# Kernel tuning notes

Measured on AMD Instinct MI355X. Metric: run time of the kernel, lower is better.

## Reference

```python
import jax, jax.numpy as jnp
import numpy as np

N = 16384
E = 524288
F_IN, F_HID, F_OUT = 128, 256, 128
EPS = 1e-5


def setup_inputs() -> dict:
    key = jax.random.key(0)
    ks = jax.random.split(key, 8)
    x = jax.random.normal(ks[0], (N, F_IN), dtype=jnp.float32)
    edge_index = jax.random.randint(ks[1], (2, E), 0, N, dtype=jnp.int64)
    edge_weight = jax.random.uniform(ks[2], (E,), dtype=jnp.float32)
    # Linear params stored as [in, out] (y = x @ W + b; same math as torch Linear)
    W1_w = jax.random.normal(ks[3], (F_IN, F_HID), dtype=jnp.float32) / np.sqrt(F_IN)
    W1_b = jnp.zeros((F_HID,), dtype=jnp.float32)
    W2_w = jax.random.normal(ks[4], (F_HID, F_OUT), dtype=jnp.float32) / np.sqrt(F_HID)
    W2_b = jnp.zeros((F_OUT,), dtype=jnp.float32)
    ln_g = jnp.ones((F_HID,), dtype=jnp.float32)
    ln_b = jnp.zeros((F_HID,), dtype=jnp.float32)
    return {"x": x, "edge_index": edge_index, "edge_weight": edge_weight,
            "W1_w": W1_w, "W1_b": W1_b, "W2_w": W2_w, "W2_b": W2_b,
            "ln_g": ln_g, "ln_b": ln_b}


def _layernorm(h, g, b):
    mu = jnp.mean(h, axis=-1, keepdims=True)
    var = jnp.var(h, axis=-1, keepdims=True)
    return (h - mu) * jax.lax.rsqrt(var + EPS) * g + b


def reference(x, edge_index, edge_weight, W1_w, W1_b, W2_w, W2_b, ln_g, ln_b):
    n = x.shape[0]
    adj = jnp.zeros((n, n), dtype=x.dtype).at[edge_index[0], edge_index[1]].set(edge_weight)
    adj = adj + jnp.eye(n, dtype=x.dtype)
    degree = jnp.clip(adj.sum(axis=1, keepdims=True), 1.0, None)
    adj = adj / degree
    h = jnp.matmul(adj, x) @ W1_w + W1_b          # [N, F_HID]
    h = jax.nn.relu(_layernorm(h, ln_g, ln_b))
    # dropout is identity in eval mode
    out = jnp.matmul(adj, h) @ W2_w + W2_b        # [N, F_OUT]
    return out
```

## Files before the change

kernel.cpp:

```cpp
#include <hip/hip_runtime.h>

#define N_NODES 16384
#define F_IN    128
#define F_HID   256
#define F_OUT   128
#define LN_EPS  1e-5f
#define CAP     128
#define HSTR    264

typedef __attribute__((ext_vector_type(8))) short bf16x8;
typedef __attribute__((ext_vector_type(4))) float f32x4;

__device__ __forceinline__ unsigned short bf16rne(float f) {
    unsigned u = __float_as_uint(f);
    unsigned r = (u + 0x7fffu + ((u >> 16) & 1u)) >> 16;
    return (unsigned short)r;
}

__global__ void prelude_kernel(const float* __restrict__ x, unsigned short* __restrict__ xb,
                               const float* __restrict__ W1, unsigned short* __restrict__ W1t,
                               const float* __restrict__ W2, unsigned short* __restrict__ W2t,
                               int* __restrict__ cur, const unsigned* __restrict__ ei,
                               int* __restrict__ mode) {
    int b = blockIdx.x, t = threadIdx.x;
    if (b < 2048) {
        int i = (b * 256 + t) * 4;
        float4 v = *(const float4*)&x[i];
        ushort4 o;
        o.x = bf16rne(v.x); o.y = bf16rne(v.y); o.z = bf16rne(v.z); o.w = bf16rne(v.w);
        *(ushort4*)&xb[i] = o;
    } else if (b < 2176) {
        int id = (b - 2048) * 256 + t;
        int n = id >> 7, k = id & 127;
        W1t[id] = bf16rne(W1[(size_t)k * F_HID + n]);
    } else if (b < 2304) {
        int id = (b - 2176) * 256 + t;
        int n = id >> 8, k = id & 255;
        W2t[id] = bf16rne(W2[(size_t)k * F_OUT + n]);
    } else if (b < 2368) {
        cur[(b - 2304) * 256 + t] = 0;
    } else {
        __shared__ int nz;
        if (t == 0) nz = 0;
        __syncthreads();
        for (int it = 0; it < 4; ++it) {
            int idx = 2 * (t + it * 256) + 1;
            if (ei[idx] != 0u) nz = 1;
        }
        __syncthreads();
        if (t == 0) *mode = (nz == 0) ? 1 : 0;
    }
}

__global__ void fill_kernel(const void* __restrict__ ei, const int* __restrict__ mode,
                            int* __restrict__ cur, int2* __restrict__ ed, int E) {
    int base = blockIdx.x * 1024 + threadIdx.x;
    int m = *mode;
#pragma unroll
    for (int u = 0; u < 4; ++u) {
        int e = base + u * 256;
        if (e >= E) continue;
        int r, c;
        if (m) {
            const long long* p = (const long long*)ei;
            r = (int)p[e]; c = (int)p[e + E];
        } else {
            const int* p = (const int*)ei;
            r = p[e]; c = p[e + E];
        }
        int pos = atomicAdd(&cur[r], 1);
        if (pos < CAP) ed[r * CAP + pos] = make_int2(c, e);
    }
}

__global__ void dedupe_kernel(const float* __restrict__ ew, int* __restrict__ cur,
                              int2* __restrict__ ed, float* __restrict__ invdeg) {
    __shared__ int scol[4][CAP];
    __shared__ int seid[4][CAP];
    int wave = threadIdx.x >> 6, lane = threadIdx.x & 63;
    int r = blockIdx.x * 4 + wave;
    int d = cur[r];
    if (d > CAP) d = CAP;
    int2* row = ed + r * CAP;
    int mycol[2], myeid[2];
    int nown = 0;
    for (int i = lane; i < d; i += 64) {
        int2 e = row[i];
        scol[wave][i] = e.x;
        seid[wave][i] = e.y;
        mycol[nown] = e.x; myeid[nown] = e.y;
        ++nown;
    }
    __syncthreads();
    float wsum = 0.0f;
    nown = 0;
    for (int i = lane; i < d; i += 64) {
        bool kill = false;
        for (int j = 0; j < d; ++j)
            if (scol[wave][j] == mycol[nown] && seid[wave][j] > myeid[nown]) { kill = true; break; }
        float w = kill ? 0.0f : ew[myeid[nown]];
        ((int*)&row[i])[1] = __float_as_int(w);
        wsum += w;
        ++nown;
    }
    for (int off = 32; off; off >>= 1) wsum += __shfl_xor(wsum, off, 64);
    if (lane == 0) {
        invdeg[r] = 1.0f / (1.0f + wsum);
        cur[r] = d;
    }
}

__global__ void spmm_bf16_kernel(const unsigned* __restrict__ xb, const int* __restrict__ cur,
                                 const int2* __restrict__ ed, const float* __restrict__ invdeg,
                                 const float* __restrict__ bias, void* __restrict__ outp,
                                 int out_bf16) {
    int wave = threadIdx.x >> 6, lane = threadIdx.x & 63;
    int r = blockIdx.x * 4 + wave;
    const int2* row = ed + r * CAP;
    int d = cur[r];
    unsigned self = xb[r * 64 + lane];
    float ax = __uint_as_float(self << 16);
    float ay = __uint_as_float(self & 0xffff0000u);
    int j = 0;
    for (; j + 8 <= d; j += 8) {
        int2 e0 = row[j],     e1 = row[j + 1], e2 = row[j + 2], e3 = row[j + 3];
        int2 e4 = row[j + 4], e5 = row[j + 5], e6 = row[j + 6], e7 = row[j + 7];
        unsigned v0 = xb[e0.x * 64 + lane];
        unsigned v1 = xb[e1.x * 64 + lane];
        unsigned v2 = xb[e2.x * 64 + lane];
        unsigned v3 = xb[e3.x * 64 + lane];
        unsigned v4 = xb[e4.x * 64 + lane];
        unsigned v5 = xb[e5.x * 64 + lane];
        unsigned v6 = xb[e6.x * 64 + lane];
        unsigned v7 = xb[e7.x * 64 + lane];
        float w0 = __int_as_float(e0.y), w1 = __int_as_float(e1.y);
        float w2 = __int_as_float(e2.y), w3 = __int_as_float(e3.y);
        float w4 = __int_as_float(e4.y), w5 = __int_as_float(e5.y);
        float w6 = __int_as_float(e6.y), w7 = __int_as_float(e7.y);
        ax += w0 * __uint_as_float(v0 << 16) + w1 * __uint_as_float(v1 << 16)
            + w2 * __uint_as_float(v2 << 16) + w3 * __uint_as_float(v3 << 16)
            + w4 * __uint_as_float(v4 << 16) + w5 * __uint_as_float(v5 << 16)
            + w6 * __uint_as_float(v6 << 16) + w7 * __uint_as_float(v7 << 16);
        ay += w0 * __uint_as_float(v0 & 0xffff0000u) + w1 * __uint_as_float(v1 & 0xffff0000u)
            + w2 * __uint_as_float(v2 & 0xffff0000u) + w3 * __uint_as_float(v3 & 0xffff0000u)
            + w4 * __uint_as_float(v4 & 0xffff0000u) + w5 * __uint_as_float(v5 & 0xffff0000u)
            + w6 * __uint_as_float(v6 & 0xffff0000u) + w7 * __uint_as_float(v7 & 0xffff0000u);
    }
    for (; j < d; ++j) {
        int2 e = row[j];
        float w = __int_as_float(e.y);
        unsigned v = xb[e.x * 64 + lane];
        ax += w * __uint_as_float(v << 16);
        ay += w * __uint_as_float(v & 0xffff0000u);
    }
    float inv = invdeg[r];
    float ox = ax * inv, oy = ay * inv;
    if (bias) { ox += bias[2 * lane]; oy += bias[2 * lane + 1]; }
    if (out_bf16) {
        unsigned pk = ((unsigned)bf16rne(oy) << 16) | (unsigned)bf16rne(ox);
        ((unsigned*)outp)[r * 64 + lane] = pk;
    } else {
        ((float2*)outp)[r * 64 + lane] = make_float2(ox, oy);
    }
}

__launch_bounds__(256)
__global__ void mlp_mfma_kernel(const unsigned short* __restrict__ h0b,
                                const unsigned short* __restrict__ W1t,
                                const unsigned short* __restrict__ W2t,
                                const float* __restrict__ b1,
                                const float* __restrict__ ln_g, const float* __restrict__ ln_b,
                                unsigned short* __restrict__ h2b) {
    __shared__ unsigned short Hs[4][16 * HSTR];
    int t = threadIdx.x;
    int wid = t >> 6, lane = t & 63;
    int lnid = lane & 15, quad = lane >> 4;
    int R = blockIdx.x * 64 + wid * 16;
    unsigned short* H = Hs[wid];

    bf16x8 a[4];
#pragma unroll
    for (int ch = 0; ch < 4; ++ch)
        a[ch] = *(const bf16x8*)&h0b[(size_t)(R + lnid) * F_IN + ch * 32 + quad * 8];
    f32x4 acc[16];
#pragma unroll
    for (int ct = 0; ct < 16; ++ct) {
        f32x4 c = {0.0f, 0.0f, 0.0f, 0.0f};
        const unsigned short* wrow = &W1t[(size_t)(ct * 16 + lnid) * F_IN];
#pragma unroll
        for (int ch = 0; ch < 4; ++ch) {
            bf16x8 b = *(const bf16x8*)&wrow[ch * 32 + quad * 8];
            c = __builtin_amdgcn_mfma_f32_16x16x32_bf16(a[ch], b, c, 0, 0, 0);
        }
        acc[ct] = c;
    }
    float s[4] = {0, 0, 0, 0}, q[4] = {0, 0, 0, 0};
#pragma unroll
    for (int ct = 0; ct < 16; ++ct) {
        float bv = b1[ct * 16 + lnid];
#pragma unroll
        for (int r = 0; r < 4; ++r) {
            float v = acc[ct][r] + bv;
            acc[ct][r] = v;
            s[r] += v; q[r] += v * v;
        }
    }
#pragma unroll
    for (int r = 0; r < 4; ++r)
        for (int off = 1; off < 16; off <<= 1) {
            s[r] += __shfl_xor(s[r], off, 64);
            q[r] += __shfl_xor(q[r], off, 64);
        }
    float mean[4], rinv[4];
#pragma unroll
    for (int r = 0; r < 4; ++r) {
        mean[r] = s[r] * (1.0f / F_HID);
        float var = q[r] * (1.0f / F_HID) - mean[r] * mean[r];
        rinv[r] = rsqrtf(var + LN_EPS);
    }
#pragma unroll
    for (int ct = 0; ct < 16; ++ct) {
        int c = ct * 16 + lnid;
        float g = ln_g[c], bb = ln_b[c];
#pragma unroll
        for (int r = 0; r < 4; ++r) {
            float v = fmaxf((acc[ct][r] - mean[r]) * rinv[r] * g + bb, 0.0f);
            H[(quad * 4 + r) * HSTR + c] = bf16rne(v);
        }
    }
    __syncthreads();

    bf16x8 a2[8];
#pragma unroll
    for (int ch = 0; ch < 8; ++ch)
        a2[ch] = *(const bf16x8*)&H[lnid * HSTR + ch * 32 + quad * 8];
#pragma unroll
    for (int ct = 0; ct < 8; ++ct) {
        f32x4 c = {0.0f, 0.0f, 0.0f, 0.0f};
        const unsigned short* wrow = &W2t[(size_t)(ct * 16 + lnid) * F_HID];
#pragma unroll
        for (int ch = 0; ch < 8; ++ch) {
            bf16x8 b = *(const bf16x8*)&wrow[ch * 32 + quad * 8];
            c = __builtin_amdgcn_mfma_f32_16x16x32_bf16(a2[ch], b, c, 0, 0, 0);
        }
#pragma unroll
        for (int r = 0; r < 4; ++r)
            H[(quad * 4 + r) * 132 + ct * 16 + lnid] = bf16rne(c[r]);
    }
    __syncthreads();

#pragma unroll
    for (int p = 0; p < 8; ++p) {
        int flat = p * 64 + lane;
        int m = flat >> 5, cg = flat & 31;
        *(ushort4*)&h2b[(size_t)(R + m) * F_OUT + cg * 4] =
            *(const ushort4*)&H[m * 132 + cg * 4];
    }
}

extern "C" void kernel_launch(void* const* d_in, const int* in_sizes, int n_in,
                              void* d_out, int out_size, void* d_ws, size_t ws_size,
                              hipStream_t stream) {
    const float* x   = (const float*)d_in[0];
    const void*  ei  = d_in[1];
    const float* ew  = (const float*)d_in[2];
    const float* W1  = (const float*)d_in[3];
    const float* b1  = (const float*)d_in[4];
    const float* W2  = (const float*)d_in[5];
    const float* b2  = (const float*)d_in[6];
    const float* lng = (const float*)d_in[7];
    const float* lnb = (const float*)d_in[8];
    float* out = (float*)d_out;
    int E = in_sizes[2];

    char* w = (char*)d_ws;
    size_t off = 0;
    auto take = [&](size_t bytes) -> char* {
        char* p = w + off;
        off += (bytes + 255) & ~(size_t)255;
        return p;
    };
    int*   cur    = (int*)take((size_t)N_NODES * 4);
    float* invdeg = (float*)take((size_t)N_NODES * 4);
    int2*  ed     = (int2*)take((size_t)N_NODES * CAP * 8);
    unsigned short* xb  = (unsigned short*)take((size_t)N_NODES * F_IN * 2);
    unsigned short* h0b = (unsigned short*)take((size_t)N_NODES * F_IN * 2);
    unsigned short* h2b = (unsigned short*)take((size_t)N_NODES * F_OUT * 2);
    unsigned short* W1t = (unsigned short*)take((size_t)F_IN * F_HID * 2);
    unsigned short* W2t = (unsigned short*)take((size_t)F_HID * F_OUT * 2);
    int*   mode   = (int*)take(4);

    prelude_kernel<<<2369, 256, 0, stream>>>(x, xb, W1, W1t, W2, W2t, cur,
                                             (const unsigned*)ei, mode);
    fill_kernel<<<(E + 1023) / 1024, 256, 0, stream>>>(ei, mode, cur, ed, E);
    dedupe_kernel<<<N_NODES / 4, 256, 0, stream>>>(ew, cur, ed, invdeg);
    spmm_bf16_kernel<<<N_NODES / 4, 256, 0, stream>>>((const unsigned*)xb, cur, ed, invdeg,
                                                      nullptr, h0b, 1);
    mlp_mfma_kernel<<<N_NODES / 64, 256, 0, stream>>>(h0b, W1t, W2t, b1, lng, lnb, h2b);
    spmm_bf16_kernel<<<N_NODES / 4, 256, 0, stream>>>((const unsigned*)h2b, cur, ed, invdeg,
                                                      b2, out, 0);
}
```

Before: 201.5 us.

## Fuse edge dedupe with first SpMM and widen gather unrolling

Merges the dedupe kernel and the first sparse aggregation into one kernel, so the row's columns and weights stay in shared memory and are reused for the gather instead of being reloaded from global memory. This also removes one kernel launch. The second SpMM becomes a dedicated kernel that reads the edge list as int4 pairs and issues 16 independent gathers per iteration for more memory-level parallelism. Adds a bounds check on edge indices in fill. The costs are extra shared memory and more registers per thread.

```diff
diff --git a/kernel.cpp b/kernel.cpp
--- a/kernel.cpp
+++ b/kernel.cpp
@@ -16,6 +16,8 @@
     unsigned r = (u + 0x7fffu + ((u >> 16) & 1u)) >> 16;
     return (unsigned short)r;
 }
+__device__ __forceinline__ float bf_lo(unsigned v) { return __uint_as_float(v << 16); }
+__device__ __forceinline__ float bf_hi(unsigned v) { return __uint_as_float(v & 0xffff0000u); }
 
 __global__ void prelude_kernel(const float* __restrict__ x, unsigned short* __restrict__ xb,
                                const float* __restrict__ W1, unsigned short* __restrict__ W1t,
@@ -68,100 +70,117 @@
             const int* p = (const int*)ei;
             r = p[e]; c = p[e + E];
         }
+        if (((unsigned)r | (unsigned)c) >= N_NODES) continue;
         int pos = atomicAdd(&cur[r], 1);
         if (pos < CAP) ed[r * CAP + pos] = make_int2(c, e);
     }
 }
 
-__global__ void dedupe_kernel(const float* __restrict__ ew, int* __restrict__ cur,
-                              int2* __restrict__ ed, float* __restrict__ invdeg) {
-    __shared__ int scol[4][CAP];
-    __shared__ int seid[4][CAP];
+__global__ void dd_spmm1_kernel(const float* __restrict__ ew, int* __restrict__ cur,
+                                int2* __restrict__ ed, float* __restrict__ invdeg,
+                                const unsigned* __restrict__ xb,
+                                unsigned* __restrict__ h0b) {
+    __shared__ int   scol[4][CAP];
+    __shared__ int   seid[4][CAP];
+    __shared__ float sw[4][CAP];
     int wave = threadIdx.x >> 6, lane = threadIdx.x & 63;
     int r = blockIdx.x * 4 + wave;
     int d = cur[r];
     if (d > CAP) d = CAP;
     int2* row = ed + r * CAP;
-    int mycol[2], myeid[2];
-    int nown = 0;
+
     for (int i = lane; i < d; i += 64) {
         int2 e = row[i];
         scol[wave][i] = e.x;
         seid[wave][i] = e.y;
-        mycol[nown] = e.x; myeid[nown] = e.y;
-        ++nown;
     }
     __syncthreads();
+
     float wsum = 0.0f;
-    nown = 0;
     for (int i = lane; i < d; i += 64) {
+        int myc = scol[wave][i], mye = seid[wave][i];
         bool kill = false;
         for (int j = 0; j < d; ++j)
-            if (scol[wave][j] == mycol[nown] && seid[wave][j] > myeid[nown]) { kill = true; break; }
-        float w = kill ? 0.0f : ew[myeid[nown]];
+            if (scol[wave][j] == myc && seid[wave][j] > mye) { kill = true; break; }
+        float w = kill ? 0.0f : ew[mye];
+        sw[wave][i] = w;
         ((int*)&row[i])[1] = __float_as_int(w);
         wsum += w;
-        ++nown;
     }
     for (int off = 32; off; off >>= 1) wsum += __shfl_xor(wsum, off, 64);
-    if (lane == 0) {
-        invdeg[r] = 1.0f / (1.0f + wsum);
-        cur[r] = d;
-    }
-}
-
-__global__ void spmm_bf16_kernel(const unsigned* __restrict__ xb, const int* __restrict__ cur,
-                                 const int2* __restrict__ ed, const float* __restrict__ invdeg,
-                                 const float* __restrict__ bias, void* __restrict__ outp,
-                                 int out_bf16) {
+    float inv = 1.0f / (1.0f + wsum);
+    if (lane == 0) { invdeg[r] = inv; cur[r] = d; }
+    __syncthreads();
+
+    unsigned self = xb[r * 64 + lane];
+    float ax = bf_lo(self), ay = bf_hi(self);
+    int j = 0;
+    for (; j + 16 <= d; j += 16) {
+        int c[16]; float w[16]; unsigned v[16];
+#pragma unroll
+        for (int u = 0; u < 16; ++u) { c[u] = scol[wave][j + u]; w[u] = sw[wave][j + u]; }
+#pragma unroll
+        for (int u = 0; u < 16; ++u) v[u] = xb[c[u] * 64 + lane];
+#pragma unroll
+        for (int u = 0; u < 16; ++u) { ax += w[u] * bf_lo(v[u]); ay += w[u] * bf_hi(v[u]); }
+    }
+    for (; j < d; ++j) {
+        int cc = scol[wave][j];
+        float w = sw[wave][j];
+        unsigned v = xb[cc * 64 + lane];
+        ax += w * bf_lo(v); ay += w * bf_hi(v);
+    }
+    float ox = ax * inv, oy = ay * inv;
+    h0b[r * 64 + lane] = ((unsigned)bf16rne(oy) << 16) | (unsigned)bf16rne(ox);
+}
+
+__global__ void spmm2_kernel(const unsigned* __restrict__ xb, const int* __restrict__ cur,
+                             const int2* __restrict__ ed, const float* __restrict__ invdeg,
+                             const float* __restrict__ bias, float* __restrict__ outp) {
     int wave = threadIdx.x >> 6, lane = threadIdx.x & 63;
     int r = blockIdx.x * 4 + wave;
-    const int2* row = ed + r * CAP;
+    const int4* rowq = (const int4*)(ed + r * CAP);
     int d = cur[r];
+    if (d > CAP) d = CAP;
     unsigned self = xb[r * 64 + lane];
-    float ax = __uint_as_float(self << 16);
-    float ay = __uint_as_float(self & 0xffff0000u);
+    float ax = bf_lo(self), ay = bf_hi(self);
     int j = 0;
-    for (; j + 8 <= d; j += 8) {
-        int2 e0 = row[j],     e1 = row[j + 1], e2 = row[j + 2], e3 = row[j + 3];
-        int2 e4 = row[j + 4], e5 = row[j + 5], e6 = row[j + 6], e7 = row[j + 7];
-        unsigned v0 = xb[e0.x * 64 + lane];
-        unsigned v1 = xb[e1.x * 64 + lane];
-        unsigned v2 = xb[e2.x * 64 + lane];
-        unsigned v3 = xb[e3.x * 64 + lane];
-        unsigned v4 = xb[e4.x * 64 + lane];
-        unsigned v5 = xb[e5.x * 64 + lane];
-        unsigned v6 = xb[e6.x * 64 + lane];
-        unsigned v7 = xb[e7.x * 64 + lane];
-        float w0 = __int_as_float(e0.y), w1 = __int_as_float(e1.y);
-        float w2 = __int_as_float(e2.y), w3 = __int_as_float(e3.y);
-        float w4 = __int_as_float(e4.y), w5 = __int_as_float(e5.y);
-        float w6 = __int_as_float(e6.y), w7 = __int_as_float(e7.y);
-        ax += w0 * __uint_as_float(v0 << 16) + w1 * __uint_as_float(v1 << 16)
-            + w2 * __uint_as_float(v2 << 16) + w3 * __uint_as_float(v3 << 16)
-            + w4 * __uint_as_float(v4 << 16) + w5 * __uint_as_float(v5 << 16)
-            + w6 * __uint_as_float(v6 << 16) + w7 * __uint_as_float(v7 << 16);
-        ay += w0 * __uint_as_float(v0 & 0xffff0000u) + w1 * __uint_as_float(v1 & 0xffff0000u)
-            + w2 * __uint_as_float(v2 & 0xffff0000u) + w3 * __uint_as_float(v3 & 0xffff0000u)
-            + w4 * __uint_as_float(v4 & 0xffff0000u) + w5 * __uint_as_float(v5 & 0xffff0000u)
-            + w6 * __uint_as_float(v6 & 0xffff0000u) + w7 * __uint_as_float(v7 & 0xffff0000u);
-    }
+    for (; j + 16 <= d; j += 16) {
+        int4 q[8]; int c[16]; float w[16]; unsigned v[16];
+#pragma unroll
+        for (int u = 0; u < 8; ++u) q[u] = rowq[(j >> 1) + u];
+#pragma unroll
+        for (int u = 0; u < 8; ++u) {
+            c[2 * u] = q[u].x;     w[2 * u] = __int_as_float(q[u].y);
+            c[2 * u + 1] = q[u].z; w[2 * u + 1] = __int_as_float(q[u].w);
+        }
+#pragma unroll
+        for (int u = 0; u < 16; ++u) v[u] = xb[c[u] * 64 + lane];
+#pragma unroll
+        for (int u = 0; u < 16; ++u) { ax += w[u] * bf_lo(v[u]); ay += w[u] * bf_hi(v[u]); }
+    }
+    for (; j + 4 <= d; j += 4) {
+        int4 q0 = rowq[j >> 1], q1 = rowq[(j >> 1) + 1];
+        unsigned v0 = xb[q0.x * 64 + lane];
+        unsigned v1 = xb[q0.z * 64 + lane];
+        unsigned v2 = xb[q1.x * 64 + lane];
+        unsigned v3 = xb[q1.z * 64 + lane];
+        float w0 = __int_as_float(q0.y), w1 = __int_as_float(q0.w);
+        float w2 = __int_as_float(q1.y), w3 = __int_as_float(q1.w);
+        ax += w0 * bf_lo(v0) + w1 * bf_lo(v1) + w2 * bf_lo(v2) + w3 * bf_lo(v3);
+        ay += w0 * bf_hi(v0) + w1 * bf_hi(v1) + w2 * bf_hi(v2) + w3 * bf_hi(v3);
+    }
+    const int2* row = (const int2*)(ed + r * CAP);
     for (; j < d; ++j) {
         int2 e = row[j];
         float w = __int_as_float(e.y);
         unsigned v = xb[e.x * 64 + lane];
-        ax += w * __uint_as_float(v << 16);
-        ay += w * __uint_as_float(v & 0xffff0000u);
+        ax += w * bf_lo(v); ay += w * bf_hi(v);
     }
     float inv = invdeg[r];
-    float ox = ax * inv, oy = ay * inv;
-    if (bias) { ox += bias[2 * lane]; oy += bias[2 * lane + 1]; }
-    if (out_bf16) {
-        unsigned pk = ((unsigned)bf16rne(oy) << 16) | (unsigned)bf16rne(ox);
-        ((unsigned*)outp)[r * 64 + lane] = pk;
-    } else {
-        ((float2*)outp)[r * 64 + lane] = make_float2(ox, oy);
-    }
+    float ox = ax * inv + bias[2 * lane];
+    float oy = ay * inv + bias[2 * lane + 1];
+    ((float2*)outp)[r * 64 + lane] = make_float2(ox, oy);
 }
 
 __launch_bounds__(256)
@@ -293,10 +312,9 @@
     prelude_kernel<<<2369, 256, 0, stream>>>(x, xb, W1, W1t, W2, W2t, cur,
                                              (const unsigned*)ei, mode);
     fill_kernel<<<(E + 1023) / 1024, 256, 0, stream>>>(ei, mode, cur, ed, E);
-    dedupe_kernel<<<N_NODES / 4, 256, 0, stream>>>(ew, cur, ed, invdeg);
-    spmm_bf16_kernel<<<N_NODES / 4, 256, 0, stream>>>((const unsigned*)xb, cur, ed, invdeg,
-                                                      nullptr, h0b, 1);
+    dd_spmm1_kernel<<<N_NODES / 4, 256, 0, stream>>>(ew, cur, ed, invdeg,
+                                                     (const unsigned*)xb, (unsigned*)h0b);
     mlp_mfma_kernel<<<N_NODES / 64, 256, 0, stream>>>(h0b, W1t, W2t, b1, lng, lnb, h2b);
-    spmm_bf16_kernel<<<N_NODES / 4, 256, 0, stream>>>((const unsigned*)h2b, cur, ed, invdeg,
-                                                      b2, out, 0);
-}
+    spmm2_kernel<<<N_NODES / 4, 256, 0, stream>>>((const unsigned*)h2b, cur, ed, invdeg,
+                                                  b2, out);
+}
```

After: 191.4 us. 5.0% less time.

## Pack edge descriptors into 32-bit col+bf16 weight and split SpMM by feature half

Applied to the files above, without the earlier changes.

Dedupe now writes a separate compact edge list where each entry holds a 16-bit column index and a bf16 weight in one 32-bit word. Each row is padded to a multiple of 16 with zero-weight self entries so the new SpMM loop can load 16 descriptors at a time without a tail loop. The SpMM is rewritten so each wave handles half of a row's features, one bf16 per lane, using twice as many blocks. The aim is to halve descriptor traffic and raise memory-level parallelism in the gather. In exchange, edge weights are rounded to bf16, per-lane loads shrink to 2 bytes, and every half-row wave reads the descriptors again.

```diff
diff --git a/kernel.cpp b/kernel.cpp
--- a/kernel.cpp
+++ b/kernel.cpp
@@ -10,16 +10,18 @@
 
 typedef __attribute__((ext_vector_type(8))) short bf16x8;
 typedef __attribute__((ext_vector_type(4))) float f32x4;
-
-__device__ __forceinline__ unsigned short bf16rne(float f) {
+typedef unsigned short u16;
+
+__device__ __forceinline__ u16 bf16rne(float f) {
     unsigned u = __float_as_uint(f);
     unsigned r = (u + 0x7fffu + ((u >> 16) & 1u)) >> 16;
-    return (unsigned short)r;
-}
-
-__global__ void prelude_kernel(const float* __restrict__ x, unsigned short* __restrict__ xb,
-                               const float* __restrict__ W1, unsigned short* __restrict__ W1t,
-                               const float* __restrict__ W2, unsigned short* __restrict__ W2t,
+    return (u16)r;
+}
+__device__ __forceinline__ float bf_lo(unsigned v) { return __uint_as_float(v << 16); }
+
+__global__ void prelude_kernel(const float* __restrict__ x, u16* __restrict__ xb,
+                               const float* __restrict__ W1, u16* __restrict__ W1t,
+                               const float* __restrict__ W2, u16* __restrict__ W2t,
                                int* __restrict__ cur, const unsigned* __restrict__ ei,
                                int* __restrict__ mode) {
     int b = blockIdx.x, t = threadIdx.x;
@@ -68,115 +70,96 @@
             const int* p = (const int*)ei;
             r = p[e]; c = p[e + E];
         }
+        if (((unsigned)r | (unsigned)c) >= N_NODES) continue;
         int pos = atomicAdd(&cur[r], 1);
         if (pos < CAP) ed[r * CAP + pos] = make_int2(c, e);
     }
 }
 
 __global__ void dedupe_kernel(const float* __restrict__ ew, int* __restrict__ cur,
-                              int2* __restrict__ ed, float* __restrict__ invdeg) {
+                              const int2* __restrict__ ed, unsigned* __restrict__ edp,
+                              float* __restrict__ invdeg) {
     __shared__ int scol[4][CAP];
     __shared__ int seid[4][CAP];
     int wave = threadIdx.x >> 6, lane = threadIdx.x & 63;
     int r = blockIdx.x * 4 + wave;
     int d = cur[r];
     if (d > CAP) d = CAP;
-    int2* row = ed + r * CAP;
-    int mycol[2], myeid[2];
-    int nown = 0;
+    int dpad = (d + 15) & ~15;
+    if (dpad > CAP) dpad = CAP;
+    const int2* row = ed + r * CAP;
     for (int i = lane; i < d; i += 64) {
         int2 e = row[i];
         scol[wave][i] = e.x;
         seid[wave][i] = e.y;
-        mycol[nown] = e.x; myeid[nown] = e.y;
-        ++nown;
     }
     __syncthreads();
     float wsum = 0.0f;
-    nown = 0;
-    for (int i = lane; i < d; i += 64) {
-        bool kill = false;
-        for (int j = 0; j < d; ++j)
-            if (scol[wave][j] == mycol[nown] && seid[wave][j] > myeid[nown]) { kill = true; break; }
-        float w = kill ? 0.0f : ew[myeid[nown]];
-        ((int*)&row[i])[1] = __float_as_int(w);
-        wsum += w;
-        ++nown;
+    unsigned* orow = edp + r * CAP;
+    for (int i = lane; i < dpad; i += 64) {
+        if (i < d) {
+            int myc = scol[wave][i], mye = seid[wave][i];
+            bool kill = false;
+            for (int j = 0; j < d; ++j)
+                if (scol[wave][j] == myc && seid[wave][j] > mye) { kill = true; break; }
+            float w = kill ? 0.0f : ew[mye];
+            wsum += w;
+            orow[i] = ((unsigned)bf16rne(w) << 16) | (unsigned)myc;
+        } else {
+            orow[i] = (unsigned)r;
+        }
     }
     for (int off = 32; off; off >>= 1) wsum += __shfl_xor(wsum, off, 64);
     if (lane == 0) {
         invdeg[r] = 1.0f / (1.0f + wsum);
-        cur[r] = d;
-    }
-}
-
-__global__ void spmm_bf16_kernel(const unsigned* __restrict__ xb, const int* __restrict__ cur,
-                                 const int2* __restrict__ ed, const float* __restrict__ invdeg,
-                                 const float* __restrict__ bias, void* __restrict__ outp,
-                                 int out_bf16) {
-    int wave = threadIdx.x >> 6, lane = threadIdx.x & 63;
-    int r = blockIdx.x * 4 + wave;
-    const int2* row = ed + r * CAP;
-    int d = cur[r];
-    unsigned self = xb[r * 64 + lane];
-    float ax = __uint_as_float(self << 16);
-    float ay = __uint_as_float(self & 0xffff0000u);
-    int j = 0;
-    for (; j + 8 <= d; j += 8) {
-        int2 e0 = row[j],     e1 = row[j + 1], e2 = row[j + 2], e3 = row[j + 3];
-        int2 e4 = row[j + 4], e5 = row[j + 5], e6 = row[j + 6], e7 = row[j + 7];
-        unsigned v0 = xb[e0.x * 64 + lane];
-        unsigned v1 = xb[e1.x * 64 + lane];
-        unsigned v2 = xb[e2.x * 64 + lane];
-        unsigned v3 = xb[e3.x * 64 + lane];
-        unsigned v4 = xb[e4.x * 64 + lane];
-        unsigned v5 = xb[e5.x * 64 + lane];
-        unsigned v6 = xb[e6.x * 64 + lane];
-        unsigned v7 = xb[e7.x * 64 + lane];
-        float w0 = __int_as_float(e0.y), w1 = __int_as_float(e1.y);
-        float w2 = __int_as_float(e2.y), w3 = __int_as_float(e3.y);
-        float w4 = __int_as_float(e4.y), w5 = __int_as_float(e5.y);
-        float w6 = __int_as_float(e6.y), w7 = __int_as_float(e7.y);
-        ax += w0 * __uint_as_float(v0 << 16) + w1 * __uint_as_float(v1 << 16)
-            + w2 * __uint_as_float(v2 << 16) + w3 * __uint_as_float(v3 << 16)
-            + w4 * __uint_as_float(v4 << 16) + w5 * __uint_as_float(v5 << 16)
-            + w6 * __uint_as_float(v6 << 16) + w7 * __uint_as_float(v7 << 16);
-        ay += w0 * __uint_as_float(v0 & 0xffff0000u) + w1 * __uint_as_float(v1 & 0xffff0000u)
-            + w2 * __uint_as_float(v2 & 0xffff0000u) + w3 * __uint_as_float(v3 & 0xffff0000u)
-            + w4 * __uint_as_float(v4 & 0xffff0000u) + w5 * __uint_as_float(v5 & 0xffff0000u)
-            + w6 * __uint_as_float(v6 & 0xffff0000u) + w7 * __uint_as_float(v7 & 0xffff0000u);
-    }
-    for (; j < d; ++j) {
-        int2 e = row[j];
-        float w = __int_as_float(e.y);
-        unsigned v = xb[e.x * 64 + lane];
-        ax += w * __uint_as_float(v << 16);
-        ay += w * __uint_as_float(v & 0xffff0000u);
-    }
-    float inv = invdeg[r];
-    float ox = ax * inv, oy = ay * inv;
-    if (bias) { ox += bias[2 * lane]; oy += bias[2 * lane + 1]; }
-    if (out_bf16) {
-        unsigned pk = ((unsigned)bf16rne(oy) << 16) | (unsigned)bf16rne(ox);
-        ((unsigned*)outp)[r * 64 + lane] = pk;
-    } else {
-        ((float2*)outp)[r * 64 + lane] = make_float2(ox, oy);
+        cur[r] = dpad;
     }
 }
 
 __launch_bounds__(256)
-__global__ void mlp_mfma_kernel(const unsigned short* __restrict__ h0b,
-                                const unsigned short* __restrict__ W1t,
-                                const unsigned short* __restrict__ W2t,
+__global__ void spmm_kernel(const u16* __restrict__ xb, const int* __restrict__ cur,
+                            const unsigned* __restrict__ edp, const float* __restrict__ invdeg,
+                            const float* __restrict__ bias, void* __restrict__ outp,
+                            int out_bf16) {
+    int wid = threadIdx.x >> 6, lane = threadIdx.x & 63;
+    int half = blockIdx.x & 1;
+    int r = __builtin_amdgcn_readfirstlane((blockIdx.x >> 1) * 4 + wid);
+    int hb = half * 64;
+    int sidx = r * F_IN + hb + lane;
+    float acc = bf_lo((unsigned)xb[sidx]);
+    int dpad = cur[r];
+    const unsigned* rowp = edp + r * CAP;
+    for (int j = 0; j < dpad; j += 16) {
+        unsigned dsc[16];
+#pragma unroll
+        for (int u = 0; u < 16; ++u) dsc[u] = rowp[j + u];
+#pragma unroll
+        for (int u = 0; u < 16; ++u) {
+            int col = (int)(dsc[u] & 0xffffu);
+            float w = __uint_as_float(dsc[u] & 0xffff0000u);
+            unsigned v = (unsigned)xb[col * F_IN + hb + lane];
+            acc += w * bf_lo(v);
+        }
+    }
+    float o = acc * invdeg[r];
+    if (bias) o += bias[hb + lane];
+    if (out_bf16) ((u16*)outp)[sidx] = bf16rne(o);
+    else          ((float*)outp)[sidx] = o;
+}
+
+__launch_bounds__(256)
+__global__ void mlp_mfma_kernel(const u16* __restrict__ h0b,
+                                const u16* __restrict__ W1t,
+                                const u16* __restrict__ W2t,
                                 const float* __restrict__ b1,
                                 const float* __restrict__ ln_g, const float* __restrict__ ln_b,
-                                unsigned short* __restrict__ h2b) {
-    __shared__ unsigned short Hs[4][16 * HSTR];
+                                u16* __restrict__ h2b) {
+    __shared__ u16 Hs[4][16 * HSTR];
     int t = threadIdx.x;
     int wid = t >> 6, lane = t & 63;
     int lnid = lane & 15, quad = lane >> 4;
     int R = blockIdx.x * 64 + wid * 16;
-    unsigned short* H = Hs[wid];
+    u16* H = Hs[wid];
 
     bf16x8 a[4];
 #pragma unroll
@@ -186,7 +169,7 @@
 #pragma unroll
     for (int ct = 0; ct < 16; ++ct) {
         f32x4 c = {0.0f, 0.0f, 0.0f, 0.0f};
-        const unsigned short* wrow = &W1t[(size_t)(ct * 16 + lnid) * F_IN];
+        const u16* wrow = &W1t[(size_t)(ct * 16 + lnid) * F_IN];
 #pragma unroll
         for (int ch = 0; ch < 4; ++ch) {
             bf16x8 b = *(const bf16x8*)&wrow[ch * 32 + quad * 8];
@@ -237,7 +220,7 @@
 #pragma unroll
     for (int ct = 0; ct < 8; ++ct) {
         f32x4 c = {0.0f, 0.0f, 0.0f, 0.0f};
-        const unsigned short* wrow = &W2t[(size_t)(ct * 16 + lnid) * F_HID];
+        const u16* wrow = &W2t[(size_t)(ct * 16 + lnid) * F_HID];
 #pragma unroll
         for (int ch = 0; ch < 8; ++ch) {
             bf16x8 b = *(const bf16x8*)&wrow[ch * 32 + quad * 8];
@@ -280,23 +263,22 @@
         off += (bytes + 255) & ~(size_t)255;
         return p;
     };
-    int*   cur    = (int*)take((size_t)N_NODES * 4);
-    float* invdeg = (float*)take((size_t)N_NODES * 4);
-    int2*  ed     = (int2*)take((size_t)N_NODES * CAP * 8);
-    unsigned short* xb  = (unsigned short*)take((size_t)N_NODES * F_IN * 2);
-    unsigned short* h0b = (unsigned short*)take((size_t)N_NODES * F_IN * 2);
-    unsigned short* h2b = (unsigned short*)take((size_t)N_NODES * F_OUT * 2);
-    unsigned short* W1t = (unsigned short*)take((size_t)F_IN * F_HID * 2);
-    unsigned short* W2t = (unsigned short*)take((size_t)F_HID * F_OUT * 2);
-    int*   mode   = (int*)take(4);
+    int*      cur    = (int*)take((size_t)N_NODES * 4);
+    float*    invdeg = (float*)take((size_t)N_NODES * 4);
+    int2*     ed     = (int2*)take((size_t)N_NODES * CAP * 8);
+    unsigned* edp    = (unsigned*)take((size_t)N_NODES * CAP * 4);
+    u16* xb  = (u16*)take((size_t)N_NODES * F_IN * 2);
+    u16* h0b = (u16*)take((size_t)N_NODES * F_IN * 2);
+    u16* h2b = (u16*)take((size_t)N_NODES * F_OUT * 2);
+    u16* W1t = (u16*)take((size_t)F_IN * F_HID * 2);
+    u16* W2t = (u16*)take((size_t)F_HID * F_OUT * 2);
+    int* mode = (int*)take(4);
 
     prelude_kernel<<<2369, 256, 0, stream>>>(x, xb, W1, W1t, W2, W2t, cur,
                                              (const unsigned*)ei, mode);
     fill_kernel<<<(E + 1023) / 1024, 256, 0, stream>>>(ei, mode, cur, ed, E);
-    dedupe_kernel<<<N_NODES / 4, 256, 0, stream>>>(ew, cur, ed, invdeg);
-    spmm_bf16_kernel<<<N_NODES / 4, 256, 0, stream>>>((const unsigned*)xb, cur, ed, invdeg,
-                                                      nullptr, h0b, 1);
+    dedupe_kernel<<<N_NODES / 4, 256, 0, stream>>>(ew, cur, ed, edp, invdeg);
+    spmm_kernel<<<N_NODES / 2, 256, 0, stream>>>(xb, cur, edp, invdeg, nullptr, h0b, 1);
     mlp_mfma_kernel<<<N_NODES / 64, 256, 0, stream>>>(h0b, W1t, W2t, b1, lng, lnb, h2b);
-    spmm_bf16_kernel<<<N_NODES / 4, 256, 0, stream>>>((const unsigned*)h2b, cur, ed, invdeg,
-                                                      b2, out, 0);
-}
+    spmm_kernel<<<N_NODES / 2, 256, 0, stream>>>(h2b, cur, edp, invdeg, b2, out, 0);
+}
```

Result: faster. 195.6 us (-2.9%).
